# Performance work log

Hardware: AMD Instinct MI355X
Metric: run time of the kernel (lower is better)

Reference implementation:

```python
import jax, jax.numpy as jnp
import numpy as np

# FP4 E2M1 value table (codes 0..7 positive, 8..15 negative, sign in MSB)
FP4_VALUES = jnp.array([0.0, 0.5, 1.0, 1.5, 2.0, 3.0, 4.0, 6.0,
                        -0.0, -0.5, -1.0, -1.5, -2.0, -3.0, -4.0, -6.0],
                       dtype=jnp.float32)


def setup_inputs() -> dict:
    key = jax.random.key(0)
    k1, k2, k3, k4 = jax.random.split(key, 4)
    O, I = 4096, 4096
    block = 16
    x = jax.random.normal(k1, (8192, I), dtype=jnp.float32)
    # packed uint4 pairs stored as int32 bytes in [0, 256)
    weight = jax.random.randint(k2, (O, I // 2), 0, 256, dtype=jnp.int32)
    # per-block FP8-style scales (positive)
    weight_scale = jax.random.uniform(k3, (O, I // block), dtype=jnp.float32, minval=0.01, maxval=1.0)
    bias = jax.random.normal(k4, (O,), dtype=jnp.float32)
    return {"x": x, "weight": weight, "weight_scale": weight_scale,
            "bias": bias, "block_size": block}


def _dequant_nvfp4(weight, weight_scale, block_size):
    # unpack two FP4 codes per byte: high nibble is the even (first) element
    hi = (weight >> 4) & 0xF
    lo = weight & 0xF
    O = weight.shape[0]
    codes = jnp.stack([hi, lo], axis=-1).reshape(O, -1)  # [O, I]
    vals = FP4_VALUES[codes]                             # [O, I] f32
    I = vals.shape[1]
    # apply per-block scale
    w = vals.reshape(O, I // block_size, block_size) * weight_scale[:, :, None]
    return w.reshape(O, I)


def reference(x, weight, weight_scale, bias, block_size):
    w = _dequant_nvfp4(weight, weight_scale, block_size)  # [O, I]
    return jnp.einsum('ti,oi->to', x, w) + bias[None, :]
```

## Files before the change

kernel.cpp:

```cpp
#include <hip/hip_runtime.h>
#include <hip/hip_fp16.h>

typedef __attribute__((ext_vector_type(8))) _Float16 f16x8;
typedef __attribute__((ext_vector_type(4))) float f32x4;

#define M_DIM 8192
#define N_DIM 4096
#define K_DIM 4096
#define BM 256
#define BN 256
#define BK 64
#define NT (K_DIM / BK)
#define ITERS (NT / 2)

__constant__ float FP4_LUT[16] = {0.f, 0.5f, 1.f, 1.5f, 2.f, 3.f, 4.f, 6.f,
                                  -0.f, -0.5f, -1.f, -1.5f, -2.f, -3.f, -4.f, -6.f};

__device__ inline void glds16(const void* g, void* l) {
    __builtin_amdgcn_global_load_lds(
        (const __attribute__((address_space(1))) void*)g,
        (__attribute__((address_space(3))) void*)l, 16, 0, 0);
}

__global__ __launch_bounds__(256) void cvt_x_kernel(const float* __restrict__ x,
                                                    _Float16* __restrict__ xh) {
    int i = (blockIdx.x * 256 + threadIdx.x) * 8;
    const float4* p = (const float4*)(x + i);
    float4 a = p[0], b = p[1];
    f16x8 h;
    h[0] = (_Float16)a.x; h[1] = (_Float16)a.y;
    h[2] = (_Float16)a.z; h[3] = (_Float16)a.w;
    h[4] = (_Float16)b.x; h[5] = (_Float16)b.y;
    h[6] = (_Float16)b.z; h[7] = (_Float16)b.w;
    *(f16x8*)(xh + i) = h;
}

__global__ __launch_bounds__(256) void dequant_w_kernel(const int* __restrict__ w,
                                                        const float* __restrict__ wsc,
                                                        _Float16* __restrict__ wh) {
    int t = blockIdx.x * 256 + threadIdx.x;
    int4 b4 = ((const int4*)w)[t];
    int o  = t >> 9;
    int j0 = (t & 511) << 2;
    float s = wsc[(o << 8) + (j0 >> 3)];
    f16x8 h;
    int b;
    b = b4.x; h[0] = (_Float16)(FP4_LUT[(b >> 4) & 15] * s); h[1] = (_Float16)(FP4_LUT[b & 15] * s);
    b = b4.y; h[2] = (_Float16)(FP4_LUT[(b >> 4) & 15] * s); h[3] = (_Float16)(FP4_LUT[b & 15] * s);
    b = b4.z; h[4] = (_Float16)(FP4_LUT[(b >> 4) & 15] * s); h[5] = (_Float16)(FP4_LUT[b & 15] * s);
    b = b4.w; h[6] = (_Float16)(FP4_LUT[(b >> 4) & 15] * s); h[7] = (_Float16)(FP4_LUT[b & 15] * s);
    *(f16x8*)(wh + ((long)o << 12) + (j0 << 1)) = h;
}


#define VM4 asm volatile("s_waitcnt vmcnt(4)" ::: "memory")
#define VM0 asm volatile("s_waitcnt vmcnt(0)" ::: "memory")
#define LG8 asm volatile("s_waitcnt lgkmcnt(8)" ::: "memory")
#define LG4 asm volatile("s_waitcnt lgkmcnt(4)" ::: "memory")
#define LG0 asm volatile("s_waitcnt lgkmcnt(0)" ::: "memory")
#define NOP ((void)0)

#define STAGE(OP, SD, KH, KOFF) do {                                           \
    _Float16* _d = lds + (SD)*32768 + (OP)*16384 + (KH)*8192 + (wid << 9);     \
    const _Float16* _s = ((OP) ? srcB : srcA) + (KOFF);                        \
    glds16(_s, _d);                                                            \
    glds16(_s + (size_t)128 * K_DIM, _d + 4096);                               \
  } while (0)

#define PH(DOAF, NCB, NKH, NMH, AFN, DOBF, BFN, LGW, MHC, AFC, BFC, STG, VMW, BAR) do { \
    STG;                                                                       \
    const _Float16* _nb = lds + (NCB)*32768 + (NKH)*8192;                      \
    if (DOAF) {                                                                \
      AFN[0] = *(const f16x8*)(_nb + a_off + (NMH)*2048);                      \
      AFN[1] = *(const f16x8*)(_nb + a_off + (NMH)*2048 + 512);                \
      AFN[2] = *(const f16x8*)(_nb + a_off + (NMH)*2048 + 1024);               \
      AFN[3] = *(const f16x8*)(_nb + a_off + (NMH)*2048 + 1536);               \
    }                                                                          \
    if (DOBF) {                                                                \
      BFN[0] = *(const f16x8*)(_nb + b_off);                                   \
      BFN[1] = *(const f16x8*)(_nb + b_off + 512);                             \
      BFN[2] = *(const f16x8*)(_nb + b_off + 1024);                            \
      BFN[3] = *(const f16x8*)(_nb + b_off + 1536);                            \
    }                                                                          \
    LGW;                                                                       \
    __builtin_amdgcn_s_setprio(1);                                             \
    _Pragma("unroll")                                                          \
    for (int mf = 0; mf < 4; ++mf) {                                           \
      _Pragma("unroll")                                                        \
      for (int nf = 0; nf < 4; ++nf)                                           \
        acc[(MHC)*4 + mf][nf] = __builtin_amdgcn_mfma_f32_16x16x32_f16(        \
            AFC[mf], BFC[nf], acc[(MHC)*4 + mf][nf], 0, 0, 0);                 \
    }                                                                          \
    __builtin_amdgcn_s_setprio(0);                                             \
    VMW;                                                                       \
    if (BAR) __builtin_amdgcn_s_barrier();                                     \
  } while (0)

__global__ __launch_bounds__(512, 2) void gemm_f16_pf(const _Float16* __restrict__ A,
                                                      const _Float16* __restrict__ B,
                                                      const float* __restrict__ bias,
                                                      float* __restrict__ C) {
    __shared__ _Float16 lds[2 * 32768];

    const int tid  = threadIdx.x;
    const int wid  = tid >> 6;
    const int lane = tid & 63;
    const int fr   = lane & 15;
    const int kg   = lane >> 4;
    const int wm   = wid >> 2;
    const int wn   = wid & 3;

    const int c = blockIdx.x & 7;
    const int q = blockIdx.x >> 3;
    const int bm = (c >> 1) * 8 + (q & 7);
    const int bn = (c & 1) * 8 + (q >> 3);
    const int brow = bm * BM;
    const int bcol = bn * BN;

    const int s_col = (((tid & 3) ^ ((tid >> 3) & 3)) << 3);
    const _Float16* srcA = A + (size_t)(brow + (tid >> 2)) * K_DIM + s_col;
    const _Float16* srcB = B + (size_t)(bcol + (tid >> 2)) * K_DIM + s_col;

    const int swz   = ((kg ^ ((fr >> 1) & 3)) << 3);
    const int a_off = (wm * 128 + fr) * 32 + swz;
    const int b_off = 16384 + (wn * 64 + fr) * 32 + swz;

    f16x8 af0[4], af1[4], bf0[4], bf1[4];
    f32x4 acc[8][4] = {};

    STAGE(0, 0, 0, 0);
    STAGE(1, 0, 0, 0);
    STAGE(0, 0, 1, 32);
    STAGE(1, 0, 1, 32);
    STAGE(0, 1, 0, 64);
    STAGE(1, 1, 0, 64);
    VM4;
    __builtin_amdgcn_s_barrier();
    af0[0] = *(const f16x8*)(lds + a_off);
    af0[1] = *(const f16x8*)(lds + a_off + 512);
    af0[2] = *(const f16x8*)(lds + a_off + 1024);
    af0[3] = *(const f16x8*)(lds + a_off + 1536);
    bf0[0] = *(const f16x8*)(lds + b_off);
    bf0[1] = *(const f16x8*)(lds + b_off + 512);
    bf0[2] = *(const f16x8*)(lds + b_off + 1024);
    bf0[3] = *(const f16x8*)(lds + b_off + 1536);

    for (int i = 0; i < ITERS - 1; ++i) {
        const int kb = i << 7;
        PH(1, 0,0,1, af1, 0,bf0, LG4, 0, af0, bf0, STAGE(0,1,1,kb+96),  NOP, 0);
        PH(1, 0,1,0, af0, 1,bf1, LG8, 1, af1, bf0, STAGE(1,1,1,kb+96),  VM4, 1);
        PH(1, 0,1,1, af1, 0,bf0, LG4, 0, af0, bf1, STAGE(0,0,0,kb+128), NOP, 0);
        PH(1, 1,0,0, af0, 1,bf0, LG8, 1, af1, bf1, STAGE(1,0,0,kb+128), VM4, 1);
        PH(1, 1,0,1, af1, 0,bf0, LG4, 0, af0, bf0, STAGE(0,0,1,kb+160), NOP, 0);
        PH(1, 1,1,0, af0, 1,bf1, LG8, 1, af1, bf0, STAGE(1,0,1,kb+160), VM4, 1);
        PH(1, 1,1,1, af1, 0,bf0, LG4, 0, af0, bf1, STAGE(0,1,0,kb+192), NOP, 0);
        PH(1, 0,0,0, af0, 1,bf0, LG8, 1, af1, bf1, STAGE(1,1,0,kb+192), VM4, 1);
    }
    {
        const int kb = (ITERS - 1) << 7;
        PH(1, 0,0,1, af1, 0,bf0, LG4, 0, af0, bf0, STAGE(0,1,1,kb+96), NOP, 0);
        PH(1, 0,1,0, af0, 1,bf1, LG8, 1, af1, bf0, STAGE(1,1,1,kb+96), VM4, 1);
        PH(1, 0,1,1, af1, 0,bf0, LG4, 0, af0, bf1, NOP,                NOP, 0);
        PH(1, 1,0,0, af0, 1,bf0, LG8, 1, af1, bf1, NOP,                VM0, 1);
        PH(1, 1,0,1, af1, 0,bf0, LG4, 0, af0, bf0, NOP,                NOP, 0);
        PH(1, 1,1,0, af0, 1,bf1, LG8, 1, af1, bf0, NOP,                NOP, 1);
        PH(1, 1,1,1, af1, 0,bf0, LG4, 0, af0, bf1, NOP,                NOP, 0);
        PH(0, 0,0,0, af0, 0,bf0, LG0, 1, af1, bf1, NOP,                NOP, 0);
    }

#pragma unroll
    for (int m = 0; m < 8; ++m) {
        int row = brow + wm * 128 + m * 16 + kg * 4;
#pragma unroll
        for (int n = 0; n < 4; ++n) {
            int col = bcol + wn * 64 + n * 16 + fr;
            float bv = bias[col];
#pragma unroll
            for (int j = 0; j < 4; ++j)
                C[(size_t)(row + j) * N_DIM + col] = acc[m][n][j] + bv;
        }
    }
}

__global__ __launch_bounds__(256) void fallback_kernel(const float* __restrict__ x,
                                                       const int* __restrict__ w,
                                                       const float* __restrict__ wsc,
                                                       const float* __restrict__ bias,
                                                       float* __restrict__ out) {
    long idx = (long)blockIdx.x * 256 + threadIdx.x;
    int t = (int)(idx >> 12);
    int o = (int)(idx & 4095);
    float acc = 0.f;
    for (int j = 0; j < K_DIM / 2; ++j) {
        int b = w[o * (K_DIM / 2) + j];
        float s = wsc[(o << 8) + (j >> 3)];
        acc += x[(long)t * K_DIM + 2 * j]     * (FP4_LUT[(b >> 4) & 15] * s);
        acc += x[(long)t * K_DIM + 2 * j + 1] * (FP4_LUT[b & 15] * s);
    }
    out[idx] = acc + bias[o];
}

extern "C" void kernel_launch(void* const* d_in, const int* in_sizes, int n_in,
                              void* d_out, int out_size, void* d_ws, size_t ws_size,
                              hipStream_t stream) {
    const float* x    = (const float*)d_in[0];
    const int*   w    = (const int*)d_in[1];
    const float* wsc  = (const float*)d_in[2];
    const float* bias = (const float*)d_in[3];
    float* out = (float*)d_out;

    const size_t xh_bytes = (size_t)M_DIM * K_DIM * 2;
    const size_t wh_bytes = (size_t)N_DIM * K_DIM * 2;

    if (ws_size >= xh_bytes + wh_bytes) {
        _Float16* xh = (_Float16*)d_ws;
        _Float16* wh = (_Float16*)((char*)d_ws + xh_bytes);
        cvt_x_kernel<<<(M_DIM * K_DIM) / (256 * 8), 256, 0, stream>>>(x, xh);
        dequant_w_kernel<<<(N_DIM * (K_DIM / 2)) / (256 * 4), 256, 0, stream>>>(w, wsc, wh);
        gemm_f16_pf<<<(M_DIM / BM) * (N_DIM / BN), 512, 0, stream>>>(xh, wh, bias, out);
    } else {
        fallback_kernel<<<((long)M_DIM * N_DIM) / 256, 256, 0, stream>>>(x, w, wsc, bias, out);
    }
}
```

Measured before the change: 279.5 us.

## Merge prep kernels and deepen LDS fragment prefetch in GEMM mainloop

The x-to-f16 conversion and FP4 weight dequant kernels become one launch that picks its role from the block index, removing one kernel launch and the gap between them. The GEMM mainloop now holds four A and four B fragment register sets, so LDS reads are issued two phases ahead and waited on with a looser lgkmcnt(12) only on barrier phases. This aims to hide LDS latency behind MFMA work, at the cost of more VGPRs, which could hurt occupancy at two blocks per CU or cause spills.

```diff
diff --git a/kernel.cpp b/kernel.cpp
--- a/kernel.cpp
+++ b/kernel.cpp
@@ -22,42 +22,42 @@
         (__attribute__((address_space(3))) void*)l, 16, 0, 0);
 }
 
-__global__ __launch_bounds__(256) void cvt_x_kernel(const float* __restrict__ x,
-                                                    _Float16* __restrict__ xh) {
-    int i = (blockIdx.x * 256 + threadIdx.x) * 8;
-    const float4* p = (const float4*)(x + i);
-    float4 a = p[0], b = p[1];
-    f16x8 h;
-    h[0] = (_Float16)a.x; h[1] = (_Float16)a.y;
-    h[2] = (_Float16)a.z; h[3] = (_Float16)a.w;
-    h[4] = (_Float16)b.x; h[5] = (_Float16)b.y;
-    h[6] = (_Float16)b.z; h[7] = (_Float16)b.w;
-    *(f16x8*)(xh + i) = h;
-}
-
-__global__ __launch_bounds__(256) void dequant_w_kernel(const int* __restrict__ w,
-                                                        const float* __restrict__ wsc,
-                                                        _Float16* __restrict__ wh) {
-    int t = blockIdx.x * 256 + threadIdx.x;
-    int4 b4 = ((const int4*)w)[t];
-    int o  = t >> 9;
-    int j0 = (t & 511) << 2;
-    float s = wsc[(o << 8) + (j0 >> 3)];
-    f16x8 h;
-    int b;
-    b = b4.x; h[0] = (_Float16)(FP4_LUT[(b >> 4) & 15] * s); h[1] = (_Float16)(FP4_LUT[b & 15] * s);
-    b = b4.y; h[2] = (_Float16)(FP4_LUT[(b >> 4) & 15] * s); h[3] = (_Float16)(FP4_LUT[b & 15] * s);
-    b = b4.z; h[4] = (_Float16)(FP4_LUT[(b >> 4) & 15] * s); h[5] = (_Float16)(FP4_LUT[b & 15] * s);
-    b = b4.w; h[6] = (_Float16)(FP4_LUT[(b >> 4) & 15] * s); h[7] = (_Float16)(FP4_LUT[b & 15] * s);
-    *(f16x8*)(wh + ((long)o << 12) + (j0 << 1)) = h;
+__global__ __launch_bounds__(256) void prep_kernel(const float* __restrict__ x,
+                                                   _Float16* __restrict__ xh,
+                                                   const int* __restrict__ w,
+                                                   const float* __restrict__ wsc,
+                                                   _Float16* __restrict__ wh) {
+    int b = blockIdx.x;
+    if (b < 16384) {
+        int i = (b * 256 + threadIdx.x) * 8;
+        const float4* p = (const float4*)(x + i);
+        float4 a = p[0], c = p[1];
+        f16x8 h;
+        h[0] = (_Float16)a.x; h[1] = (_Float16)a.y;
+        h[2] = (_Float16)a.z; h[3] = (_Float16)a.w;
+        h[4] = (_Float16)c.x; h[5] = (_Float16)c.y;
+        h[6] = (_Float16)c.z; h[7] = (_Float16)c.w;
+        *(f16x8*)(xh + i) = h;
+    } else {
+        int t = (b - 16384) * 256 + threadIdx.x;
+        int4 b4 = ((const int4*)w)[t];
+        int o  = t >> 9;
+        int j0 = (t & 511) << 2;
+        float s = wsc[(o << 8) + (j0 >> 3)];
+        f16x8 h;
+        int v;
+        v = b4.x; h[0] = (_Float16)(FP4_LUT[(v >> 4) & 15] * s); h[1] = (_Float16)(FP4_LUT[v & 15] * s);
+        v = b4.y; h[2] = (_Float16)(FP4_LUT[(v >> 4) & 15] * s); h[3] = (_Float16)(FP4_LUT[v & 15] * s);
+        v = b4.z; h[4] = (_Float16)(FP4_LUT[(v >> 4) & 15] * s); h[5] = (_Float16)(FP4_LUT[v & 15] * s);
+        v = b4.w; h[6] = (_Float16)(FP4_LUT[(v >> 4) & 15] * s); h[7] = (_Float16)(FP4_LUT[v & 15] * s);
+        *(f16x8*)(wh + ((long)o << 12) + (j0 << 1)) = h;
+    }
 }
 
 
 #define VM4 asm volatile("s_waitcnt vmcnt(4)" ::: "memory")
 #define VM0 asm volatile("s_waitcnt vmcnt(0)" ::: "memory")
-#define LG8 asm volatile("s_waitcnt lgkmcnt(8)" ::: "memory")
-#define LG4 asm volatile("s_waitcnt lgkmcnt(4)" ::: "memory")
-#define LG0 asm volatile("s_waitcnt lgkmcnt(0)" ::: "memory")
+#define LG12 asm volatile("s_waitcnt lgkmcnt(12)" ::: "memory")
 #define NOP ((void)0)
 
 #define STAGE(OP, SD, KH, KOFF) do {                                           \
@@ -67,20 +67,21 @@
     glds16(_s + (size_t)128 * K_DIM, _d + 4096);                               \
   } while (0)
 
-#define PH(DOAF, NCB, NKH, NMH, AFN, DOBF, BFN, LGW, MHC, AFC, BFC, STG, VMW, BAR) do { \
+#define PH(DOA, AFD, ACB, AKH, AMH, DOB, BFD, BCB, BKH, MHC, AFC, BFC, STG, LGW, VMW, BAR) do { \
     STG;                                                                       \
-    const _Float16* _nb = lds + (NCB)*32768 + (NKH)*8192;                      \
-    if (DOAF) {                                                                \
-      AFN[0] = *(const f16x8*)(_nb + a_off + (NMH)*2048);                      \
-      AFN[1] = *(const f16x8*)(_nb + a_off + (NMH)*2048 + 512);                \
-      AFN[2] = *(const f16x8*)(_nb + a_off + (NMH)*2048 + 1024);               \
-      AFN[3] = *(const f16x8*)(_nb + a_off + (NMH)*2048 + 1536);               \
+    if (DOA) {                                                                 \
+      const _Float16* _na = lds + (ACB)*32768 + (AKH)*8192;                    \
+      AFD[0] = *(const f16x8*)(_na + a_off + (AMH)*2048);                      \
+      AFD[1] = *(const f16x8*)(_na + a_off + (AMH)*2048 + 512);                \
+      AFD[2] = *(const f16x8*)(_na + a_off + (AMH)*2048 + 1024);               \
+      AFD[3] = *(const f16x8*)(_na + a_off + (AMH)*2048 + 1536);               \
     }                                                                          \
-    if (DOBF) {                                                                \
-      BFN[0] = *(const f16x8*)(_nb + b_off);                                   \
-      BFN[1] = *(const f16x8*)(_nb + b_off + 512);                             \
-      BFN[2] = *(const f16x8*)(_nb + b_off + 1024);                            \
-      BFN[3] = *(const f16x8*)(_nb + b_off + 1536);                            \
+    if (DOB) {                                                                 \
+      const _Float16* _nb = lds + (BCB)*32768 + (BKH)*8192;                    \
+      BFD[0] = *(const f16x8*)(_nb + b_off);                                   \
+      BFD[1] = *(const f16x8*)(_nb + b_off + 512);                             \
+      BFD[2] = *(const f16x8*)(_nb + b_off + 1024);                            \
+      BFD[3] = *(const f16x8*)(_nb + b_off + 1536);                            \
     }                                                                          \
     LGW;                                                                       \
     __builtin_amdgcn_s_setprio(1);                                             \
@@ -125,7 +126,7 @@
     const int a_off = (wm * 128 + fr) * 32 + swz;
     const int b_off = 16384 + (wn * 64 + fr) * 32 + swz;
 
-    f16x8 af0[4], af1[4], bf0[4], bf1[4];
+    f16x8 af0[4], af1[4], af2[4], af3[4], bf0[4], bf1[4], bf2[4], bf3[4];
     f32x4 acc[8][4] = {};
 
     STAGE(0, 0, 0, 0);
@@ -140,6 +141,10 @@
     af0[1] = *(const f16x8*)(lds + a_off + 512);
     af0[2] = *(const f16x8*)(lds + a_off + 1024);
     af0[3] = *(const f16x8*)(lds + a_off + 1536);
+    af1[0] = *(const f16x8*)(lds + a_off + 2048);
+    af1[1] = *(const f16x8*)(lds + a_off + 2560);
+    af1[2] = *(const f16x8*)(lds + a_off + 3072);
+    af1[3] = *(const f16x8*)(lds + a_off + 3584);
     bf0[0] = *(const f16x8*)(lds + b_off);
     bf0[1] = *(const f16x8*)(lds + b_off + 512);
     bf0[2] = *(const f16x8*)(lds + b_off + 1024);
@@ -147,25 +152,25 @@
 
     for (int i = 0; i < ITERS - 1; ++i) {
         const int kb = i << 7;
-        PH(1, 0,0,1, af1, 0,bf0, LG4, 0, af0, bf0, STAGE(0,1,1,kb+96),  NOP, 0);
-        PH(1, 0,1,0, af0, 1,bf1, LG8, 1, af1, bf0, STAGE(1,1,1,kb+96),  VM4, 1);
-        PH(1, 0,1,1, af1, 0,bf0, LG4, 0, af0, bf1, STAGE(0,0,0,kb+128), NOP, 0);
-        PH(1, 1,0,0, af0, 1,bf0, LG8, 1, af1, bf1, STAGE(1,0,0,kb+128), VM4, 1);
-        PH(1, 1,0,1, af1, 0,bf0, LG4, 0, af0, bf0, STAGE(0,0,1,kb+160), NOP, 0);
-        PH(1, 1,1,0, af0, 1,bf1, LG8, 1, af1, bf0, STAGE(1,0,1,kb+160), VM4, 1);
-        PH(1, 1,1,1, af1, 0,bf0, LG4, 0, af0, bf1, STAGE(0,1,0,kb+192), NOP, 0);
-        PH(1, 0,0,0, af0, 1,bf0, LG8, 1, af1, bf1, STAGE(1,1,0,kb+192), VM4, 1);
+        PH(1, af2, 0,1,0, 1, bf1, 0,1, 0, af0, bf0, STAGE(0,1,1,kb+96),  NOP, NOP, 0);
+        PH(1, af3, 0,1,1, 0, bf0, 0,0, 1, af1, bf0, STAGE(1,1,1,kb+96),  LG12, VM4, 1);
+        PH(1, af0, 1,0,0, 1, bf2, 1,0, 0, af2, bf1, STAGE(0,0,0,kb+128), NOP, NOP, 0);
+        PH(1, af1, 1,0,1, 0, bf0, 0,0, 1, af3, bf1, STAGE(1,0,0,kb+128), LG12, VM4, 1);
+        PH(1, af2, 1,1,0, 1, bf3, 1,1, 0, af0, bf2, STAGE(0,0,1,kb+160), NOP, NOP, 0);
+        PH(1, af3, 1,1,1, 0, bf0, 0,0, 1, af1, bf2, STAGE(1,0,1,kb+160), LG12, VM4, 1);
+        PH(1, af0, 0,0,0, 1, bf0, 0,0, 0, af2, bf3, STAGE(0,1,0,kb+192), NOP, NOP, 0);
+        PH(1, af1, 0,0,1, 0, bf0, 0,0, 1, af3, bf3, STAGE(1,1,0,kb+192), LG12, VM4, 1);
     }
     {
         const int kb = (ITERS - 1) << 7;
-        PH(1, 0,0,1, af1, 0,bf0, LG4, 0, af0, bf0, STAGE(0,1,1,kb+96), NOP, 0);
-        PH(1, 0,1,0, af0, 1,bf1, LG8, 1, af1, bf0, STAGE(1,1,1,kb+96), VM4, 1);
-        PH(1, 0,1,1, af1, 0,bf0, LG4, 0, af0, bf1, NOP,                NOP, 0);
-        PH(1, 1,0,0, af0, 1,bf0, LG8, 1, af1, bf1, NOP,                VM0, 1);
-        PH(1, 1,0,1, af1, 0,bf0, LG4, 0, af0, bf0, NOP,                NOP, 0);
-        PH(1, 1,1,0, af0, 1,bf1, LG8, 1, af1, bf0, NOP,                NOP, 1);
-        PH(1, 1,1,1, af1, 0,bf0, LG4, 0, af0, bf1, NOP,                NOP, 0);
-        PH(0, 0,0,0, af0, 0,bf0, LG0, 1, af1, bf1, NOP,                NOP, 0);
+        PH(1, af2, 0,1,0, 1, bf1, 0,1, 0, af0, bf0, STAGE(0,1,1,kb+96), NOP, NOP, 0);
+        PH(1, af3, 0,1,1, 0, bf0, 0,0, 1, af1, bf0, STAGE(1,1,1,kb+96), LG12, VM4, 1);
+        PH(1, af0, 1,0,0, 1, bf2, 1,0, 0, af2, bf1, NOP,                NOP, NOP, 0);
+        PH(1, af1, 1,0,1, 0, bf0, 0,0, 1, af3, bf1, NOP,                LG12, VM0, 1);
+        PH(1, af2, 1,1,0, 1, bf3, 1,1, 0, af0, bf2, NOP,                NOP, NOP, 0);
+        PH(1, af3, 1,1,1, 0, bf0, 0,0, 1, af1, bf2, NOP,                LG12, NOP, 1);
+        PH(0, af0, 0,0,0, 0, bf0, 0,0, 0, af2, bf3, NOP,                NOP, NOP, 0);
+        PH(0, af0, 0,0,0, 0, bf0, 0,0, 1, af3, bf3, NOP,                NOP, NOP, 0);
     }
 
 #pragma unroll
@@ -215,8 +220,7 @@
     if (ws_size >= xh_bytes + wh_bytes) {
         _Float16* xh = (_Float16*)d_ws;
         _Float16* wh = (_Float16*)((char*)d_ws + xh_bytes);
-        cvt_x_kernel<<<(M_DIM * K_DIM) / (256 * 8), 256, 0, stream>>>(x, xh);
-        dequant_w_kernel<<<(N_DIM * (K_DIM / 2)) / (256 * 4), 256, 0, stream>>>(w, wsc, wh);
+        prep_kernel<<<16384 + 8192, 256, 0, stream>>>(x, xh, w, wsc, wh);
         gemm_f16_pf<<<(M_DIM / BM) * (N_DIM / BN), 512, 0, stream>>>(xh, wh, bias, out);
     } else {
         fallback_kernel<<<((long)M_DIM * N_DIM) / 256, 256, 0, stream>>>(x, w, wsc, bias, out);
```

After: 299.1 us. 1.07x slower.
